# Kernel optimization log

Measured on AMD Instinct MI355X. Metric: run time of the kernel, lower is better.

## Reference

```python
import jax, jax.numpy as jnp
import numpy as np

SR = 16000
FRAME_LENGTH = 64
ATTENUATE_GAIN = 0.04


def upsample_linear(x, scale):
    """torch nn.Upsample(mode='linear', align_corners=False) along last axis."""
    L = x.shape[-1]
    Lo = L * scale
    src = (jnp.arange(Lo, dtype=x.dtype) + 0.5) / scale - 0.5
    src = jnp.maximum(src, 0.0)  # torch clamps negative source coords to 0
    i0 = jnp.floor(src).astype(jnp.int32)
    i1 = jnp.minimum(i0 + 1, L - 1)
    w = src - i0.astype(x.dtype)
    return jnp.take(x, i0, axis=-1) * (1.0 - w) + jnp.take(x, i1, axis=-1) * w


def setup_inputs() -> dict:
    key = jax.random.key(0)
    k1, k2, k3, k4, k5 = jax.random.split(key, 5)
    batch, poly, harm, frames = 2, 8, 64, 500
    # fundamentals in a musical range (~30..1030 Hz) so the anti-alias mask is nontrivial
    f0 = jax.random.uniform(k1, (batch, poly, frames), dtype=jnp.float32) * 1000.0 + 30.0
    c = jax.random.uniform(k2, (batch, poly, harm, frames), dtype=jnp.float32)
    v = jax.random.uniform(k3, (batch, poly, frames), dtype=jnp.float32)
    a = jax.random.uniform(k4, (batch, frames), dtype=jnp.float32)
    random_phases = jax.random.uniform(k5, (batch, poly * harm, 1), dtype=jnp.float32)
    return {"f0": f0, "c": c, "v": v, "a": a, "random_phases": random_phases}


def reference(f0, c, v, a, random_phases):
    batch, poly, harm, frames = c.shape
    num_osc = poly * harm
    partial_mult = jnp.arange(1, harm + 1, dtype=jnp.float32)  # (harm,)

    # (batch, poly, harm, frames)
    f0_bank = f0[:, :, None, :] * partial_mult[None, None, :, None]
    v_bank = jnp.broadcast_to(v[:, :, None, :], (batch, poly, harm, frames))

    f0_bank = f0_bank.reshape(batch, num_osc, frames)
    c_bank = c.reshape(batch, num_osc, frames)
    v_bank = v_bank.reshape(batch, num_osc, frames)

    mask = (f0_bank < SR / 2).astype(jnp.float32)
    c_bank = c_bank * mask

    f0_up = upsample_linear(f0_bank, FRAME_LENGTH)          # (b, osc, audio)
    phase = jnp.cumsum(f0_up / SR, axis=2) + random_phases   # (b, osc, audio)
    a_up = upsample_linear(c_bank, FRAME_LENGTH)
    v_up = upsample_linear(v_bank, FRAME_LENGTH)

    sinusoid_bank = jnp.sin(2.0 * np.pi * phase) * ATTENUATE_GAIN * a_up * v_up

    # loudness is upsampled in the original forward but unused in the output
    _ = upsample_linear(a[None], FRAME_LENGTH)[0]

    return jnp.sum(sinusoid_bank, axis=1)  # (batch, audio)
```

## Files before the change

kernel.cpp:

```cpp
#include <hip/hip_runtime.h>
#include <math.h>

#define SR_I 16000
#define FRAMES 500
#define UP 64
#define AUDIO (FRAMES * UP)
#define POLY 8
#define HARM 64
#define NYQ 8000.0f

__global__ __launch_bounds__(512) void k_fused(const float* __restrict__ f0,
                                               const float* __restrict__ cc,
                                               const float* __restrict__ vv,
                                               const float* __restrict__ rp,
                                               float* __restrict__ out) {
    __shared__ float4 quads[POLY][2][HARM];
    __shared__ float part[POLY][UP];

    const int blk = blockIdx.x;
    const int b = blk / FRAMES;
    const int t = blk - b * FRAMES;
    const int tid = threadIdx.x;
    const int p = tid >> 6;
    const int k = tid & 63;
    const bool lowhalf = (k < 32);

    const int tm = max(t - 1, 0);
    const int tp = min(t + 1, FRAMES - 1);

    const int bpi = b * POLY + p;
    const float* f0p = f0 + bpi * FRAMES;
    const float* vp  = vv + bpi * FRAMES;
    const float* cp  = cc + (size_t)bpi * HARM * FRAMES;

    const float craw_m = cp[k * FRAMES + tm];
    const float craw_c = cp[k * FRAMES + t];
    const float craw_p = cp[k * FRAMES + tp];
    const float rpl    = rp[bpi * HARM + k];

    float pre[8];
    #pragma unroll
    for (int u = 0; u < 8; ++u) {
        const int j = k + u * 64;
        pre[u] = (j < t) ? f0p[j] : 0.0f;
    }

    const float A = f0p[tm];
    const float B = f0p[t];
    const float C = f0p[tp];
    const float vA = vp[tm];
    const float vB = vp[t];
    const float vC = vp[tp];

    const float nf = (float)(k + 1);
    const bool mA = (nf * A < NYQ);
    const bool mB = (nf * B < NYQ);
    const bool mC = (nf * C < NYQ);
    const float cA = mA ? craw_m : 0.0f;
    const float cB = mB ? craw_c : 0.0f;
    const float cC = mC ? craw_p : 0.0f;
    quads[p][0][k] = make_float4(cA, cB, rpl, 0.0f);
    quads[p][1][k] = make_float4(cB, cC, rpl, 0.0f);

    const unsigned long long bal = __ballot(mA || mB || mC);
    int hmax = (int)__popcll(bal);
    hmax = (hmax + 3) & ~3;

    double ssum = 0.0;
    #pragma unroll
    for (int u = 0; u < 8; ++u) ssum += (double)pre[u];
    #pragma unroll
    for (int off = 32; off; off >>= 1)
        ssum += __shfl_xor(ssum, off, 64);
    const double dA = (double)A, dB = (double)B, dC = (double)C;
    const double Pfr = (64.0 * ssum + 8.0 * (dB - dA)) * (1.0 / (double)SR_I);

    double S;
    if (lowhalf) {
        const double kk = (double)k;
        S = ((kk + 1.0) * dA
             + (dB - dA) * (kk * (kk + 1.0) * 0.5 + 32.5 * (kk + 1.0)) * (1.0 / 64.0))
            * (1.0 / (double)SR_I);
    } else {
        const double qq = (double)(k - 32);
        S = (8.0 * dA + 24.0 * dB) * (1.0 / (double)SR_I)
            + ((qq + 1.0) * dB + (dC - dB) * (qq + 1.0) * (qq + 1.0) * (1.0 / 128.0))
              * (1.0 / (double)SR_I);
    }
    const double Phi = Pfr + S;
    const float phi = (float)(Phi - floor(Phi));

    const float w = (lowhalf ? ((float)k + 32.5f) : ((float)k - 31.5f)) * (1.0f / 64.0f);
    const float w1 = 1.0f - w;
    const float v0 = lowhalf ? vA : vB;
    const float v1 = lowhalf ? vB : vC;
    const float vup04 = 0.04f * (w1 * v0 + w * v1);
    const float W0 = w1 * vup04;
    const float W1 = w * vup04;

    const float4* qb = &quads[p][lowhalf ? 0 : 1][0];

    float acc0 = 0.0f, acc1 = 0.0f, acc2 = 0.0f, acc3 = 0.0f;
    float nf0 = 1.0f, nf1 = 2.0f, nf2 = 3.0f, nf3 = 4.0f;

    for (int n0 = 1; n0 <= hmax; n0 += 4) {
        const float4 qa = qb[n0 - 1];
        const float4 qc = qb[n0 + 0];
        const float4 qd = qb[n0 + 1];
        const float4 qe = qb[n0 + 2];

        {
            const float cup = fmaf(W1, qa.y, W0 * qa.x);
            const float ph  = fmaf(nf0, phi, qa.z);
            acc0 = fmaf(cup, __builtin_amdgcn_sinf(__builtin_amdgcn_fractf(ph)), acc0);
        }
        {
            const float cup = fmaf(W1, qc.y, W0 * qc.x);
            const float ph  = fmaf(nf1, phi, qc.z);
            acc1 = fmaf(cup, __builtin_amdgcn_sinf(__builtin_amdgcn_fractf(ph)), acc1);
        }
        {
            const float cup = fmaf(W1, qd.y, W0 * qd.x);
            const float ph  = fmaf(nf2, phi, qd.z);
            acc2 = fmaf(cup, __builtin_amdgcn_sinf(__builtin_amdgcn_fractf(ph)), acc2);
        }
        {
            const float cup = fmaf(W1, qe.y, W0 * qe.x);
            const float ph  = fmaf(nf3, phi, qe.z);
            acc3 = fmaf(cup, __builtin_amdgcn_sinf(__builtin_amdgcn_fractf(ph)), acc3);
        }
        nf0 += 4.0f; nf1 += 4.0f; nf2 += 4.0f; nf3 += 4.0f;
    }

    part[p][k] = (acc0 + acc1) + (acc2 + acc3);
    __syncthreads();
    if (tid < 64) {
        float sum = 0.0f;
        #pragma unroll
        for (int q = 0; q < POLY; ++q) sum += part[q][tid];
        out[(size_t)b * AUDIO + t * UP + tid] = sum;
    }
}

extern "C" void kernel_launch(void* const* d_in, const int* in_sizes, int n_in,
                              void* d_out, int out_size, void* d_ws, size_t ws_size,
                              hipStream_t stream) {
    const float* f0 = (const float*)d_in[0];
    const float* c  = (const float*)d_in[1];
    const float* v  = (const float*)d_in[2];
    const float* rp = (const float*)d_in[4];
    float* out = (float*)d_out;

    k_fused<<<2 * FRAMES, 512, 0, stream>>>(f0, c, v, rp, out);
}
```

Before: 17.22 us.

## Pre-transpose harmonic amplitudes to frame-major layout for coalesced loads

Adds a separate transpose kernel that rewrites c from (batch, osc, frames) into a (batch, frames, osc) workspace buffer through a padded shared-memory tile. The main kernel then reads the three amplitude samples per oscillator contiguously across lanes instead of with a stride of FRAMES. This removes strided, uncoalesced global loads in the fused kernel. In exchange it adds a second kernel launch and an extra full read and write of c.

```diff
diff --git a/kernel.cpp b/kernel.cpp
--- a/kernel.cpp
+++ b/kernel.cpp
@@ -8,9 +8,39 @@
 #define POLY 8
 #define HARM 64
 #define NYQ 8000.0f
+#define NOSC (POLY * HARM)
+
+__global__ __launch_bounds__(256) void k_transpose(const float* __restrict__ cc,
+                                                   float* __restrict__ cT) {
+    __shared__ float tile[64][65];
+    const int blk = blockIdx.x;
+    const int chunk = blk & 7;
+    const int bp = blk >> 3;
+    const int tc = chunk * 64;
+    const int w = threadIdx.x >> 6;
+    const int l = threadIdx.x & 63;
+
+    const float* src = cc + (size_t)bp * HARM * FRAMES;
+
+    #pragma unroll
+    for (int i = 0; i < 16; ++i) {
+        const int r = w * 16 + i;
+        const int t = tc + l;
+        tile[r][l] = (t < FRAMES) ? src[r * FRAMES + t] : 0.0f;
+    }
+    __syncthreads();
+    const int b = bp >> 3, p = bp & 7;
+    #pragma unroll
+    for (int i = 0; i < 16; ++i) {
+        const int tl = w * 16 + i;
+        const int t = tc + tl;
+        if (t < FRAMES)
+            cT[(size_t)(b * FRAMES + t) * NOSC + p * HARM + l] = tile[l][tl];
+    }
+}
 
 __global__ __launch_bounds__(512) void k_fused(const float* __restrict__ f0,
-                                               const float* __restrict__ cc,
+                                               const float* __restrict__ cT,
                                                const float* __restrict__ vv,
                                                const float* __restrict__ rp,
                                                float* __restrict__ out) {
@@ -31,11 +61,11 @@
     const int bpi = b * POLY + p;
     const float* f0p = f0 + bpi * FRAMES;
     const float* vp  = vv + bpi * FRAMES;
-    const float* cp  = cc + (size_t)bpi * HARM * FRAMES;
 
-    const float craw_m = cp[k * FRAMES + tm];
-    const float craw_c = cp[k * FRAMES + t];
-    const float craw_p = cp[k * FRAMES + tp];
+    const float* cTb = cT + (size_t)b * FRAMES * NOSC + p * HARM + k;
+    const float craw_m = cTb[(size_t)tm * NOSC];
+    const float craw_c = cTb[(size_t)t  * NOSC];
+    const float craw_p = cTb[(size_t)tp * NOSC];
     const float rpl    = rp[bpi * HARM + k];
 
     float pre[8];
@@ -151,5 +181,8 @@
     const float* rp = (const float*)d_in[4];
     float* out = (float*)d_out;
 
-    k_fused<<<2 * FRAMES, 512, 0, stream>>>(f0, c, v, rp, out);
+    float* cT = (float*)d_ws;
+
+    k_transpose<<<2 * POLY * 8, 256, 0, stream>>>(c, cT);
+    k_fused<<<2 * FRAMES, 512, 0, stream>>>(f0, cT, v, rp, out);
 }
```

Measured after the change: 21.28 us. +23.6%, slower.

## Balance harmonic work across waves by striping harmonic quads over all polyphonic voices

Applied to the files above, without the earlier changes.

Previously each wave synthesized every harmonic of one voice, so the block waited on the voice with the most harmonics below Nyquist. Now each wave writes its phase and weights plus its per-voice harmonic count to shared memory. After a block barrier, each wave processes a rotated pair of 4-harmonic slices from every voice, which spreads the work evenly across the eight waves. This costs an extra __syncthreads and more LDS reads for per-voice phase and weight data.

```diff
diff --git a/kernel.cpp b/kernel.cpp
--- a/kernel.cpp
+++ b/kernel.cpp
@@ -15,20 +15,22 @@
                                                const float* __restrict__ rp,
                                                float* __restrict__ out) {
     __shared__ float4 quads[POLY][2][HARM];
+    __shared__ float4 phiW[POLY][UP];
     __shared__ float part[POLY][UP];
+    __shared__ int hmaxs[POLY];
 
     const int blk = blockIdx.x;
     const int b = blk / FRAMES;
     const int t = blk - b * FRAMES;
     const int tid = threadIdx.x;
-    const int p = tid >> 6;
+    const int wv = tid >> 6;
     const int k = tid & 63;
     const bool lowhalf = (k < 32);
 
     const int tm = max(t - 1, 0);
     const int tp = min(t + 1, FRAMES - 1);
 
-    const int bpi = b * POLY + p;
+    const int bpi = b * POLY + wv;
     const float* f0p = f0 + bpi * FRAMES;
     const float* vp  = vv + bpi * FRAMES;
     const float* cp  = cc + (size_t)bpi * HARM * FRAMES;
@@ -56,15 +58,13 @@
     const bool mA = (nf * A < NYQ);
     const bool mB = (nf * B < NYQ);
     const bool mC = (nf * C < NYQ);
-    const float cA = mA ? craw_m : 0.0f;
-    const float cB = mB ? craw_c : 0.0f;
-    const float cC = mC ? craw_p : 0.0f;
-    quads[p][0][k] = make_float4(cA, cB, rpl, 0.0f);
-    quads[p][1][k] = make_float4(cB, cC, rpl, 0.0f);
+    quads[wv][0][k] = make_float4(mA ? craw_m : 0.0f, mB ? craw_c : 0.0f, rpl, 0.0f);
+    quads[wv][1][k] = make_float4(mB ? craw_c : 0.0f, mC ? craw_p : 0.0f, rpl, 0.0f);
 
     const unsigned long long bal = __ballot(mA || mB || mC);
     int hmax = (int)__popcll(bal);
     hmax = (hmax + 3) & ~3;
+    if (k == 0) hmaxs[wv] = hmax;
 
     double ssum = 0.0;
     #pragma unroll
@@ -95,44 +95,52 @@
     const float v0 = lowhalf ? vA : vB;
     const float v1 = lowhalf ? vB : vC;
     const float vup04 = 0.04f * (w1 * v0 + w * v1);
-    const float W0 = w1 * vup04;
-    const float W1 = w * vup04;
+    phiW[wv][k] = make_float4(phi, w1 * vup04, w * vup04, 0.0f);
 
-    const float4* qb = &quads[p][lowhalf ? 0 : 1][0];
+    __syncthreads();
 
+    const int half = lowhalf ? 0 : 1;
     float acc0 = 0.0f, acc1 = 0.0f, acc2 = 0.0f, acc3 = 0.0f;
-    float nf0 = 1.0f, nf1 = 2.0f, nf2 = 3.0f, nf3 = 4.0f;
 
-    for (int n0 = 1; n0 <= hmax; n0 += 4) {
-        const float4 qa = qb[n0 - 1];
-        const float4 qc = qb[n0 + 0];
-        const float4 qd = qb[n0 + 1];
-        const float4 qe = qb[n0 + 2];
-
+    auto do_quad = [&](const float4* q4, float base, const float4& pw) {
+        const float4 qa = q4[0], qc = q4[1], qd = q4[2], qe = q4[3];
         {
-            const float cup = fmaf(W1, qa.y, W0 * qa.x);
-            const float ph  = fmaf(nf0, phi, qa.z);
+            const float cup = fmaf(pw.z, qa.y, pw.y * qa.x);
+            const float ph  = fmaf(base + 1.0f, pw.x, qa.z);
             acc0 = fmaf(cup, __builtin_amdgcn_sinf(__builtin_amdgcn_fractf(ph)), acc0);
         }
         {
-            const float cup = fmaf(W1, qc.y, W0 * qc.x);
-            const float ph  = fmaf(nf1, phi, qc.z);
+            const float cup = fmaf(pw.z, qc.y, pw.y * qc.x);
+            const float ph  = fmaf(base + 2.0f, pw.x, qc.z);
             acc1 = fmaf(cup, __builtin_amdgcn_sinf(__builtin_amdgcn_fractf(ph)), acc1);
         }
         {
-            const float cup = fmaf(W1, qd.y, W0 * qd.x);
-            const float ph  = fmaf(nf2, phi, qd.z);
+            const float cup = fmaf(pw.z, qd.y, pw.y * qd.x);
+            const float ph  = fmaf(base + 3.0f, pw.x, qd.z);
             acc2 = fmaf(cup, __builtin_amdgcn_sinf(__builtin_amdgcn_fractf(ph)), acc2);
         }
         {
-            const float cup = fmaf(W1, qe.y, W0 * qe.x);
-            const float ph  = fmaf(nf3, phi, qe.z);
+            const float cup = fmaf(pw.z, qe.y, pw.y * qe.x);
+            const float ph  = fmaf(base + 4.0f, pw.x, qe.z);
             acc3 = fmaf(cup, __builtin_amdgcn_sinf(__builtin_amdgcn_fractf(ph)), acc3);
         }
-        nf0 += 4.0f; nf1 += 4.0f; nf2 += 4.0f; nf3 += 4.0f;
+    };
+
+    #pragma unroll
+    for (int pv = 0; pv < POLY; ++pv) {
+        const int sA = (wv + pv) & 7;
+        const int hm = hmaxs[pv];
+        if (sA * 4 < hm) {
+            const float4 pw = phiW[pv][k];
+            const float4* qb = &quads[pv][half][0];
+            do_quad(qb + 4 * sA, (float)(4 * sA), pw);
+            const int sB = sA + 8;
+            if (sB * 4 < hm)
+                do_quad(qb + 4 * sB, (float)(4 * sB), pw);
+        }
     }
 
-    part[p][k] = (acc0 + acc1) + (acc2 + acc3);
+    part[wv][k] = (acc0 + acc1) + (acc2 + acc3);
     __syncthreads();
     if (tid < 64) {
         float sum = 0.0f;
```

New measurement: 17.74 us. +3.0%, slower.

## Process two frames per block to share loads and prefix-sum work

Applied to the files above, without the earlier changes.

Each block now handles two consecutive frames instead of one, halving the grid to 500 blocks. The f0 prefix sum, coefficient/velocity loads and setup are computed once and reused for both frames, and two sinusoid loops run back to back per thread. This amortizes per-block setup and global loads, at the cost of fewer blocks (less parallelism across CUs) and more registers and LDS per block.

```diff
diff --git a/kernel.cpp b/kernel.cpp
--- a/kernel.cpp
+++ b/kernel.cpp
@@ -14,57 +14,67 @@
                                                const float* __restrict__ vv,
                                                const float* __restrict__ rp,
                                                float* __restrict__ out) {
-    __shared__ float4 quads[POLY][2][HARM];
-    __shared__ float part[POLY][UP];
+    __shared__ float4 quads[2][POLY][2][HARM];
+    __shared__ float part[2][POLY][UP];
 
     const int blk = blockIdx.x;
-    const int b = blk / FRAMES;
-    const int t = blk - b * FRAMES;
+    const int b = blk / (FRAMES / 2);
+    const int g = blk - b * (FRAMES / 2);
+    const int t0 = 2 * g;
+    const int t1 = t0 + 1;
     const int tid = threadIdx.x;
     const int p = tid >> 6;
     const int k = tid & 63;
     const bool lowhalf = (k < 32);
 
-    const int tm = max(t - 1, 0);
-    const int tp = min(t + 1, FRAMES - 1);
+    const int tm = max(t0 - 1, 0);
+    const int tq = min(t0 + 2, FRAMES - 1);
 
     const int bpi = b * POLY + p;
     const float* f0p = f0 + bpi * FRAMES;
     const float* vp  = vv + bpi * FRAMES;
     const float* cp  = cc + (size_t)bpi * HARM * FRAMES;
 
-    const float craw_m = cp[k * FRAMES + tm];
-    const float craw_c = cp[k * FRAMES + t];
-    const float craw_p = cp[k * FRAMES + tp];
-    const float rpl    = rp[bpi * HARM + k];
+    const float cm = cp[k * FRAMES + tm];
+    const float cb = cp[k * FRAMES + t0];
+    const float cx = cp[k * FRAMES + t1];
+    const float cd = cp[k * FRAMES + tq];
+    const float rpl = rp[bpi * HARM + k];
 
     float pre[8];
     #pragma unroll
     for (int u = 0; u < 8; ++u) {
         const int j = k + u * 64;
-        pre[u] = (j < t) ? f0p[j] : 0.0f;
+        pre[u] = (j < t0) ? f0p[j] : 0.0f;
     }
 
     const float A = f0p[tm];
-    const float B = f0p[t];
-    const float C = f0p[tp];
+    const float B = f0p[t0];
+    const float C = f0p[t1];
+    const float D = f0p[tq];
     const float vA = vp[tm];
-    const float vB = vp[t];
-    const float vC = vp[tp];
+    const float vB = vp[t0];
+    const float vC = vp[t1];
+    const float vD = vp[tq];
 
     const float nf = (float)(k + 1);
     const bool mA = (nf * A < NYQ);
     const bool mB = (nf * B < NYQ);
     const bool mC = (nf * C < NYQ);
-    const float cA = mA ? craw_m : 0.0f;
-    const float cB = mB ? craw_c : 0.0f;
-    const float cC = mC ? craw_p : 0.0f;
-    quads[p][0][k] = make_float4(cA, cB, rpl, 0.0f);
-    quads[p][1][k] = make_float4(cB, cC, rpl, 0.0f);
+    const bool mD = (nf * D < NYQ);
+    const float qA = mA ? cm : 0.0f;
+    const float qB = mB ? cb : 0.0f;
+    const float qC = mC ? cx : 0.0f;
+    const float qD = mD ? cd : 0.0f;
+    quads[0][p][0][k] = make_float4(qA, qB, rpl, 0.0f);
+    quads[0][p][1][k] = make_float4(qB, qC, rpl, 0.0f);
+    quads[1][p][0][k] = make_float4(qB, qC, rpl, 0.0f);
+    quads[1][p][1][k] = make_float4(qC, qD, rpl, 0.0f);
 
-    const unsigned long long bal = __ballot(mA || mB || mC);
-    int hmax = (int)__popcll(bal);
-    hmax = (hmax + 3) & ~3;
+    int hm0 = (int)__popcll(__ballot(mA || mB || mC));
+    int hm1 = (int)__popcll(__ballot(mB || mC || mD));
+    hm0 = (hm0 + 3) & ~3;
+    hm1 = (hm1 + 3) & ~3;
 
     double ssum = 0.0;
     #pragma unroll
@@ -72,73 +82,87 @@
     #pragma unroll
     for (int off = 32; off; off >>= 1)
         ssum += __shfl_xor(ssum, off, 64);
-    const double dA = (double)A, dB = (double)B, dC = (double)C;
-    const double Pfr = (64.0 * ssum + 8.0 * (dB - dA)) * (1.0 / (double)SR_I);
+    const double dA = (double)A, dB = (double)B, dC = (double)C, dD = (double)D;
+    const double Pfr0 = (64.0 * ssum + 8.0 * (dB - dA)) * (1.0 / (double)SR_I);
+    const double Pfr1 = (64.0 * (ssum + dB) + 8.0 * (dC - dB)) * (1.0 / (double)SR_I);
 
-    double S;
+    const double kk = (double)k;
+    const double qq = (double)(k - 32);
+    double S0, S1;
     if (lowhalf) {
-        const double kk = (double)k;
-        S = ((kk + 1.0) * dA
-             + (dB - dA) * (kk * (kk + 1.0) * 0.5 + 32.5 * (kk + 1.0)) * (1.0 / 64.0))
-            * (1.0 / (double)SR_I);
+        const double lin = (kk * (kk + 1.0) * 0.5 + 32.5 * (kk + 1.0)) * (1.0 / 64.0);
+        S0 = ((kk + 1.0) * dA + (dB - dA) * lin) * (1.0 / (double)SR_I);
+        S1 = ((kk + 1.0) * dB + (dC - dB) * lin) * (1.0 / (double)SR_I);
     } else {
-        const double qq = (double)(k - 32);
-        S = (8.0 * dA + 24.0 * dB) * (1.0 / (double)SR_I)
-            + ((qq + 1.0) * dB + (dC - dB) * (qq + 1.0) * (qq + 1.0) * (1.0 / 128.0))
-              * (1.0 / (double)SR_I);
+        const double sq = (qq + 1.0) * (qq + 1.0) * (1.0 / 128.0);
+        S0 = (8.0 * dA + 24.0 * dB + (qq + 1.0) * dB + (dC - dB) * sq) * (1.0 / (double)SR_I);
+        S1 = (8.0 * dB + 24.0 * dC + (qq + 1.0) * dC + (dD - dC) * sq) * (1.0 / (double)SR_I);
     }
-    const double Phi = Pfr + S;
-    const float phi = (float)(Phi - floor(Phi));
+    const double Phi0 = Pfr0 + S0;
+    const double Phi1 = Pfr1 + S1;
+    const float phi0 = (float)(Phi0 - floor(Phi0));
+    const float phi1 = (float)(Phi1 - floor(Phi1));
 
     const float w = (lowhalf ? ((float)k + 32.5f) : ((float)k - 31.5f)) * (1.0f / 64.0f);
     const float w1 = 1.0f - w;
-    const float v0 = lowhalf ? vA : vB;
-    const float v1 = lowhalf ? vB : vC;
-    const float vup04 = 0.04f * (w1 * v0 + w * v1);
-    const float W0 = w1 * vup04;
-    const float W1 = w * vup04;
+    const float v00 = lowhalf ? vA : vB;
+    const float v01 = lowhalf ? vB : vC;
+    const float v10 = lowhalf ? vB : vC;
+    const float v11 = lowhalf ? vC : vD;
+    const float vu0 = 0.04f * (w1 * v00 + w * v01);
+    const float vu1 = 0.04f * (w1 * v10 + w * v11);
 
-    const float4* qb = &quads[p][lowhalf ? 0 : 1][0];
+    const int half = lowhalf ? 0 : 1;
 
-    float acc0 = 0.0f, acc1 = 0.0f, acc2 = 0.0f, acc3 = 0.0f;
-    float nf0 = 1.0f, nf1 = 2.0f, nf2 = 3.0f, nf3 = 4.0f;
+    #pragma unroll
+    for (int f = 0; f < 2; ++f) {
+        const int hmax = f ? hm1 : hm0;
+        const float phi = f ? phi1 : phi0;
+        const float W0 = (f ? vu1 : vu0) * w1;
+        const float W1 = (f ? vu1 : vu0) * w;
+        const float4* qb = &quads[f][p][half][0];
 
-    for (int n0 = 1; n0 <= hmax; n0 += 4) {
-        const float4 qa = qb[n0 - 1];
-        const float4 qc = qb[n0 + 0];
-        const float4 qd = qb[n0 + 1];
-        const float4 qe = qb[n0 + 2];
+        float acc0 = 0.0f, acc1 = 0.0f, acc2 = 0.0f, acc3 = 0.0f;
+        float nf0 = 1.0f, nf1 = 2.0f, nf2 = 3.0f, nf3 = 4.0f;
 
-        {
-            const float cup = fmaf(W1, qa.y, W0 * qa.x);
-            const float ph  = fmaf(nf0, phi, qa.z);
-            acc0 = fmaf(cup, __builtin_amdgcn_sinf(__builtin_amdgcn_fractf(ph)), acc0);
+        for (int n0 = 1; n0 <= hmax; n0 += 4) {
+            const float4 qa = qb[n0 - 1];
+            const float4 qc = qb[n0 + 0];
+            const float4 qd = qb[n0 + 1];
+            const float4 qe = qb[n0 + 2];
+            {
+                const float cup = fmaf(W1, qa.y, W0 * qa.x);
+                const float ph  = fmaf(nf0, phi, qa.z);
+                acc0 = fmaf(cup, __builtin_amdgcn_sinf(__builtin_amdgcn_fractf(ph)), acc0);
+            }
+            {
+                const float cup = fmaf(W1, qc.y, W0 * qc.x);
+                const float ph  = fmaf(nf1, phi, qc.z);
+                acc1 = fmaf(cup, __builtin_amdgcn_sinf(__builtin_amdgcn_fractf(ph)), acc1);
+            }
+            {
+                const float cup = fmaf(W1, qd.y, W0 * qd.x);
+                const float ph  = fmaf(nf2, phi, qd.z);
+                acc2 = fmaf(cup, __builtin_amdgcn_sinf(__builtin_amdgcn_fractf(ph)), acc2);
+            }
+            {
+                const float cup = fmaf(W1, qe.y, W0 * qe.x);
+                const float ph  = fmaf(nf3, phi, qe.z);
+                acc3 = fmaf(cup, __builtin_amdgcn_sinf(__builtin_amdgcn_fractf(ph)), acc3);
+            }
+            nf0 += 4.0f; nf1 += 4.0f; nf2 += 4.0f; nf3 += 4.0f;
         }
-        {
-            const float cup = fmaf(W1, qc.y, W0 * qc.x);
-            const float ph  = fmaf(nf1, phi, qc.z);
-            acc1 = fmaf(cup, __builtin_amdgcn_sinf(__builtin_amdgcn_fractf(ph)), acc1);
-        }
-        {
-            const float cup = fmaf(W1, qd.y, W0 * qd.x);
-            const float ph  = fmaf(nf2, phi, qd.z);
-            acc2 = fmaf(cup, __builtin_amdgcn_sinf(__builtin_amdgcn_fractf(ph)), acc2);
-        }
-        {
-            const float cup = fmaf(W1, qe.y, W0 * qe.x);
-            const float ph  = fmaf(nf3, phi, qe.z);
-            acc3 = fmaf(cup, __builtin_amdgcn_sinf(__builtin_amdgcn_fractf(ph)), acc3);
-        }
-        nf0 += 4.0f; nf1 += 4.0f; nf2 += 4.0f; nf3 += 4.0f;
+        part[f][p][k] = (acc0 + acc1) + (acc2 + acc3);
     }
 
-    part[p][k] = (acc0 + acc1) + (acc2 + acc3);
     __syncthreads();
-    if (tid < 64) {
+    if (tid < 128) {
+        const int f = tid >> 6;
+        const int j = tid & 63;
         float sum = 0.0f;
         #pragma unroll
-        for (int q = 0; q < POLY; ++q) sum += part[q][tid];
-        out[(size_t)b * AUDIO + t * UP + tid] = sum;
+        for (int q = 0; q < POLY; ++q) sum += part[f][q][j];
+        out[(size_t)b * AUDIO + (t0 + f) * UP + j] = sum;
     }
 }
 
@@ -151,5 +175,5 @@
     const float* rp = (const float*)d_in[4];
     float* out = (float*)d_out;
 
-    k_fused<<<2 * FRAMES, 512, 0, stream>>>(f0, c, v, rp, out);
+    k_fused<<<2 * (FRAMES / 2), 512, 0, stream>>>(f0, c, v, rp, out);
 }
```

Result: faster. 16.86 us (-2.1%).
